# Kernel tuning notes

Hardware: AMD Instinct MI355X
Metric: run time of the kernel (lower is better)

## Reference

```python
import jax, jax.numpy as jnp
import numpy as np
import math

D_MODEL = 1024
N_HEADS = 16
D_HEAD = D_MODEL // N_HEADS
BIAS_HIDDEN = 32
B, N = 2, 1024


def setup_inputs() -> dict:
    key = jax.random.key(0)
    ks = jax.random.split(key, 16)
    s = 1.0 / math.sqrt(D_MODEL)
    inp = {
        "x": jax.random.normal(ks[0], (B, N, D_MODEL), dtype=jnp.float32),
        "xyz": jax.random.normal(ks[1], (B, N, 3), dtype=jnp.float32),
        "Wq": jax.random.normal(ks[2], (D_MODEL, D_MODEL), jnp.float32) * s,
        "bq": jnp.zeros((D_MODEL,), jnp.float32),
        "Wk": jax.random.normal(ks[3], (D_MODEL, D_MODEL), jnp.float32) * s,
        "bk": jnp.zeros((D_MODEL,), jnp.float32),
        "Wv": jax.random.normal(ks[4], (D_MODEL, D_MODEL), jnp.float32) * s,
        "bv": jnp.zeros((D_MODEL,), jnp.float32),
        "Wo": jax.random.normal(ks[5], (D_MODEL, D_MODEL), jnp.float32) * s,
        "bo": jnp.zeros((D_MODEL,), jnp.float32),
        "W1": jax.random.normal(ks[6], (3, BIAS_HIDDEN), jnp.float32) * (1.0 / math.sqrt(3.0)),
        "b1": jnp.zeros((BIAS_HIDDEN,), jnp.float32),
        "W2": jax.random.normal(ks[7], (BIAS_HIDDEN, N_HEADS), jnp.float32) * (1.0 / math.sqrt(BIAS_HIDDEN)),
        "b2": jnp.zeros((N_HEADS,), jnp.float32),
    }
    return inp


def reference(x, xyz, Wq, bq, Wk, bk, Wv, bv, Wo, bo, W1, b1, W2, b2):
    Bv, Nv, _ = x.shape
    # q,k,v projections -> [B, H, N, Dh]
    def proj(W, b):
        return (x @ W + b).reshape(Bv, Nv, N_HEADS, D_HEAD).transpose(0, 2, 1, 3)
    q = proj(Wq, bq)
    k = proj(Wk, bk)
    v = proj(Wv, bv)
    scores = jnp.einsum('bhid,bhjd->bhij', q, k) / math.sqrt(D_HEAD)
    # pairwise relative positions -> per-head bias via tiny MLP
    rel_pos = xyz[:, :, None, :] - xyz[:, None, :, :]            # [B,N,N,3]
    hidden = jax.nn.relu(rel_pos @ W1 + b1)                      # [B,N,N,hid]
    bias = (hidden @ W2 + b2).transpose(0, 3, 1, 2)              # [B,H,N,N]
    attn = jax.nn.softmax(scores + bias, axis=-1)                # [B,H,N,N]
    out = jnp.einsum('bhij,bhjd->bhid', attn, v)                 # [B,H,N,Dh]
    out = out.transpose(0, 2, 1, 3).reshape(Bv, Nv, D_MODEL)
    out = out @ Wo + bo
    return (out, attn)
```

## Files before the change

kernel.cpp:

```cpp
#include <hip/hip_runtime.h>
#include <hip/hip_bf16.h>
#include <math.h>

#define NTOK   1024
#define DMODEL 1024
#define NHEADS 16
#define DHEAD  64

typedef __attribute__((ext_vector_type(8))) short short8;
typedef __attribute__((ext_vector_type(4))) float floatx4;
#define MFMA(a,b,c) __builtin_amdgcn_mfma_f32_16x16x32_bf16(a,b,c,0,0,0)

__device__ __forceinline__ void bf16_split(float f, ushort& h, ushort& l) {
    unsigned u = __float_as_uint(f);
    unsigned hr = (u + 0x7FFFu + ((u >> 16) & 1u)) >> 16;
    h = (ushort)hr;
    float fh = __uint_as_float(hr << 16);
    float res = f - fh;
    unsigned u2 = __float_as_uint(res);
    l = (ushort)((u2 + 0x7FFFu + ((u2 >> 16) & 1u)) >> 16);
}

__device__ __forceinline__ int swzK(int r) { return (r & 7) ^ ((r >> 3) & 7); }

__global__ __launch_bounds__(256) void bias_kernel(
    const float* __restrict__ xyz,
    const float* __restrict__ W1, const float* __restrict__ b1,
    const float* __restrict__ W2, const float* __restrict__ b2,
    float* __restrict__ attnO)
{
    __shared__ float wbuf[656];
    int tid = threadIdx.x;
    for (int i = tid; i < 656; i += 256) {
        float v;
        if (i < 96)       v = W1[i];
        else if (i < 128) v = b1[i - 96];
        else if (i < 640) v = W2[i - 128];
        else              v = b2[i - 640];
        wbuf[i] = v;
    }
    __syncthreads();
    const float* w1s = wbuf;
    const float* b1s = wbuf + 96;
    const float* w2s = wbuf + 128;
    const float* b2s = wbuf + 640;

    int j = blockIdx.x * 256 + tid;
    int i = blockIdx.y;
    int b = blockIdx.z;

    float xi0 = xyz[((size_t)b * NTOK + i) * 3 + 0];
    float xi1 = xyz[((size_t)b * NTOK + i) * 3 + 1];
    float xi2 = xyz[((size_t)b * NTOK + i) * 3 + 2];
    float d0 = xi0 - xyz[((size_t)b * NTOK + j) * 3 + 0];
    float d1 = xi1 - xyz[((size_t)b * NTOK + j) * 3 + 1];
    float d2 = xi2 - xyz[((size_t)b * NTOK + j) * 3 + 2];

    float h[32];
#pragma unroll
    for (int hh = 0; hh < 32; ++hh) {
        float v = b1s[hh] + d0 * w1s[hh] + d1 * w1s[32 + hh] + d2 * w1s[64 + hh];
        h[hh] = fmaxf(v, 0.f);
    }
    size_t base = (size_t)b * NHEADS * 1048576 + (size_t)i * 1024 + j;
#pragma unroll
    for (int hd = 0; hd < NHEADS; ++hd) {
        float acc = b2s[hd];
#pragma unroll
        for (int hh = 0; hh < 32; ++hh) acc += h[hh] * w2s[hh * 16 + hd];
        attnO[base + (size_t)hd * 1048576] = acc;
    }
}

__global__ __launch_bounds__(256) void convx_kernel(
    const float* __restrict__ x, ushort* __restrict__ xh, ushort* __restrict__ xl)
{
    int id = blockIdx.x * 256 + threadIdx.x;
    float4 v = ((const float4*)x)[id];
    ushort h0,h1,h2,h3,l0,l1,l2,l3;
    bf16_split(v.x,h0,l0); bf16_split(v.y,h1,l1);
    bf16_split(v.z,h2,l2); bf16_split(v.w,h3,l3);
    ushort4 hv; hv.x=h0; hv.y=h1; hv.z=h2; hv.w=h3;
    ushort4 lv; lv.x=l0; lv.y=l1; lv.z=l2; lv.w=l3;
    ((ushort4*)xh)[id] = hv;
    ((ushort4*)xl)[id] = lv;
}

__global__ __launch_bounds__(256) void convw_kernel(
    const float* __restrict__ Wq, const float* __restrict__ Wk,
    const float* __restrict__ Wv, const float* __restrict__ Wo,
    ushort* __restrict__ Wcth, ushort* __restrict__ Wctl,
    ushort* __restrict__ Woth, ushort* __restrict__ Wotl)
{
    __shared__ float t[64][65];
    int z = blockIdx.z;
    const float* W = (z == 0) ? Wq : (z == 1) ? Wk : (z == 2) ? Wv : Wo;
    int n0 = blockIdx.x * 64, k0 = blockIdx.y * 64;
    int tid = threadIdx.x;
    int c4 = tid & 15, rr = tid >> 4;
#pragma unroll
    for (int t4 = 0; t4 < 4; ++t4) {
        int row = rr + t4 * 16;
        float4 v = *(const float4*)&W[(size_t)(k0 + row) * 1024 + n0 + c4 * 4];
        t[row][c4 * 4 + 0] = v.x; t[row][c4 * 4 + 1] = v.y;
        t[row][c4 * 4 + 2] = v.z; t[row][c4 * 4 + 3] = v.w;
    }
    __syncthreads();
    ushort* oh = (z < 3) ? Wcth : Woth;
    ushort* ol = (z < 3) ? Wctl : Wotl;
    int nbase = (z < 3) ? z * 1024 : 0;
#pragma unroll
    for (int t4 = 0; t4 < 4; ++t4) {
        int nl = rr + t4 * 16;
        int kk = c4 * 4;
        ushort4 hv, lv;
        ushort h, l;
        bf16_split(t[kk + 0][nl], h, l); hv.x = h; lv.x = l;
        bf16_split(t[kk + 1][nl], h, l); hv.y = h; lv.y = l;
        bf16_split(t[kk + 2][nl], h, l); hv.z = h; lv.z = l;
        bf16_split(t[kk + 3][nl], h, l); hv.w = h; lv.w = l;
        size_t o = (size_t)(nbase + n0 + nl) * 1024 + k0 + kk;
        *(ushort4*)&oh[o] = hv;
        *(ushort4*)&ol[o] = lv;
    }
}

__global__ __launch_bounds__(256) void mm_kernel(
    const ushort* __restrict__ Ah, const ushort* __restrict__ Al,
    const ushort* __restrict__ Bh, const ushort* __restrict__ Bl,
    const float* __restrict__ bq, const float* __restrict__ bk,
    const float* __restrict__ bv,
    float* __restrict__ out,
    ushort* __restrict__ qh, ushort* __restrict__ ql,
    ushort* __restrict__ kh, ushort* __restrict__ kl,
    ushort* __restrict__ vth, ushort* __restrict__ vtl,
    int mode)
{
    __shared__ ushort lds[4][64][64];

    int n0 = blockIdx.x * 64;
    int m0 = blockIdx.y * 64;
    int w = threadIdx.x >> 6, l = threadIdx.x & 63;
    int li = l & 15, lg = l >> 4;
    int wm = w >> 1, wn = w & 1;

    const ushort* gbase;
    if      (w == 0) gbase = Ah + (size_t)m0 * 1024;
    else if (w == 1) gbase = Al + (size_t)m0 * 1024;
    else if (w == 2) gbase = Bh + (size_t)n0 * 1024;
    else             gbase = Bl + (size_t)n0 * 1024;
    ushort* lbase = &lds[w][0][0];
    int srow = l >> 3;
    int sc   = l & 7;

    floatx4 acc[2][2];
#pragma unroll
    for (int i = 0; i < 2; ++i)
#pragma unroll
        for (int j = 0; j < 2; ++j) acc[i][j] = (floatx4){0.f, 0.f, 0.f, 0.f};

    for (int ks = 0; ks < 16; ++ks) {
        int k0 = ks * 64;
#pragma unroll
        for (int t = 0; t < 8; ++t) {
            int rl = t * 8 + srow;
            int cs = sc ^ swzK(rl);
            const ushort* g = gbase + (size_t)rl * 1024 + k0 + cs * 8;
            __builtin_amdgcn_global_load_lds(
                (const __attribute__((address_space(1))) unsigned int*)g,
                (__attribute__((address_space(3))) unsigned int*)(lbase + t * 512),
                16, 0, 0);
        }
        __syncthreads();
#pragma unroll
        for (int kk = 0; kk < 2; ++kk) {
            short8 a[2][2], b2[2][2];
#pragma unroll
            for (int f = 0; f < 2; ++f) {
                int ra = wm * 32 + f * 16 + li;
                int ca = ((kk * 4 + lg) ^ swzK(ra)) * 8;
                a[f][0] = *(const short8*)&lds[0][ra][ca];
                a[f][1] = *(const short8*)&lds[1][ra][ca];
                int rb = wn * 32 + f * 16 + li;
                int cb = ((kk * 4 + lg) ^ swzK(rb)) * 8;
                b2[f][0] = *(const short8*)&lds[2][rb][cb];
                b2[f][1] = *(const short8*)&lds[3][rb][cb];
            }
#pragma unroll
            for (int fm = 0; fm < 2; ++fm)
#pragma unroll
                for (int fn = 0; fn < 2; ++fn) {
                    acc[fm][fn] = MFMA(a[fm][0], b2[fn][0], acc[fm][fn]);
                    acc[fm][fn] = MFMA(a[fm][0], b2[fn][1], acc[fm][fn]);
                    acc[fm][fn] = MFMA(a[fm][1], b2[fn][0], acc[fm][fn]);
                }
        }
        __syncthreads();
    }

    if (mode == 0) {
#pragma unroll
        for (int fm = 0; fm < 2; ++fm)
#pragma unroll
            for (int fn = 0; fn < 2; ++fn) {
                int col = n0 + wn * 32 + fn * 16 + li;
                float bval = bq[col];
#pragma unroll
                for (int r = 0; r < 4; ++r) {
                    int row = m0 + wm * 32 + fm * 16 + lg * 4 + r;
                    out[(size_t)row * 1024 + col] = acc[fm][fn][r] + bval;
                }
            }
    } else {
        int z = n0 >> 10;
        const float* bp = (z == 0) ? bq : (z == 1) ? bk : bv;
#pragma unroll
        for (int fm = 0; fm < 2; ++fm)
#pragma unroll
            for (int fn = 0; fn < 2; ++fn) {
                int col = n0 + wn * 32 + fn * 16 + li;
                int nloc = col & 1023;
                int hd = nloc >> 6, d = nloc & 63;
                float bval = bp[nloc];
#pragma unroll
                for (int r = 0; r < 4; ++r) {
                    int row = m0 + wm * 32 + fm * 16 + lg * 4 + r;
                    int b = row >> 10, nn = row & 1023;
                    int bh = b * NHEADS + hd;
                    float v = acc[fm][fn][r] + bval;
                    ushort h, lo; bf16_split(v, h, lo);
                    if (z == 0) {
                        size_t o = ((size_t)bh * NTOK + nn) * DHEAD + d;
                        qh[o] = h; ql[o] = lo;
                    } else if (z == 1) {
                        size_t o = ((size_t)bh * NTOK + nn) * DHEAD + d;
                        kh[o] = h; kl[o] = lo;
                    } else {
                        size_t o = ((size_t)bh * DHEAD + d) * NTOK + nn;
                        vth[o] = h; vtl[o] = lo;
                    }
                }
            }
    }
}

__global__ __launch_bounds__(256) void score_kernel(
    const ushort* __restrict__ qh, const ushort* __restrict__ ql,
    const ushort* __restrict__ kh, const ushort* __restrict__ kl,
    float* __restrict__ attnO)
{
    __shared__ float redM[4][16];
    __shared__ float redS[4][16];
    int qt = blockIdx.x, hd = blockIdx.y, b = blockIdx.z;
    int bh = b * NHEADS + hd;
    int w = threadIdx.x >> 6, l = threadIdx.x & 63;
    int li = l & 15, lg = l >> 4;

    size_t qoff = ((size_t)bh * NTOK + qt * 16 + li) * DHEAD + lg * 8;
    short8 q0h = *(const short8*)(qh + qoff);
    short8 q0l = *(const short8*)(ql + qoff);
    short8 q1h = *(const short8*)(qh + qoff + 32);
    short8 q1l = *(const short8*)(ql + qoff + 32);

    floatx4 acc[16];
#pragma unroll
    for (int jf = 0; jf < 16; ++jf) acc[jf] = (floatx4){0.f, 0.f, 0.f, 0.f};

    int jbase = w * 256;
#pragma unroll
    for (int jf = 0; jf < 16; ++jf) {
        size_t koff = ((size_t)bh * NTOK + jbase + jf * 16 + li) * DHEAD + lg * 8;
        short8 K0h = *(const short8*)(kh + koff);
        short8 K0l = *(const short8*)(kl + koff);
        short8 K1h = *(const short8*)(kh + koff + 32);
        short8 K1l = *(const short8*)(kl + koff + 32);
        acc[jf] = MFMA(q0h, K0h, acc[jf]);
        acc[jf] = MFMA(q0h, K0l, acc[jf]);
        acc[jf] = MFMA(q0l, K0h, acc[jf]);
        acc[jf] = MFMA(q1h, K1h, acc[jf]);
        acc[jf] = MFMA(q1h, K1l, acc[jf]);
        acc[jf] = MFMA(q1l, K1h, acc[jf]);
    }

    float* prow = attnO + ((size_t)bh * NTOK + qt * 16) * NTOK;

    float mloc[4] = {-1e30f, -1e30f, -1e30f, -1e30f};
#pragma unroll
    for (int jf = 0; jf < 16; ++jf)
#pragma unroll
        for (int r = 0; r < 4; ++r) {
            float s = acc[jf][r] * 0.125f
                    + prow[(size_t)(lg * 4 + r) * NTOK + jbase + jf * 16 + li];
            acc[jf][r] = s;
            mloc[r] = fmaxf(mloc[r], s);
        }
#pragma unroll
    for (int r = 0; r < 4; ++r) {
        float m = mloc[r];
        m = fmaxf(m, __shfl_xor(m, 1, 64));
        m = fmaxf(m, __shfl_xor(m, 2, 64));
        m = fmaxf(m, __shfl_xor(m, 4, 64));
        m = fmaxf(m, __shfl_xor(m, 8, 64));
        mloc[r] = m;
    }
    if (li == 0) {
#pragma unroll
        for (int r = 0; r < 4; ++r) redM[w][lg * 4 + r] = mloc[r];
    }
    __syncthreads();
    float M[4];
#pragma unroll
    for (int r = 0; r < 4; ++r) {
        int row = lg * 4 + r;
        M[r] = fmaxf(fmaxf(redM[0][row], redM[1][row]),
                     fmaxf(redM[2][row], redM[3][row]));
    }
    float sloc[4] = {0.f, 0.f, 0.f, 0.f};
#pragma unroll
    for (int jf = 0; jf < 16; ++jf)
#pragma unroll
        for (int r = 0; r < 4; ++r) {
            float e = __expf(acc[jf][r] - M[r]);
            acc[jf][r] = e;
            sloc[r] += e;
        }
#pragma unroll
    for (int r = 0; r < 4; ++r) {
        float s = sloc[r];
        s += __shfl_xor(s, 1, 64);
        s += __shfl_xor(s, 2, 64);
        s += __shfl_xor(s, 4, 64);
        s += __shfl_xor(s, 8, 64);
        sloc[r] = s;
    }
    if (li == 0) {
#pragma unroll
        for (int r = 0; r < 4; ++r) redS[w][lg * 4 + r] = sloc[r];
    }
    __syncthreads();
    float inv[4];
#pragma unroll
    for (int r = 0; r < 4; ++r) {
        int row = lg * 4 + r;
        inv[r] = 1.0f / (redS[0][row] + redS[1][row] + redS[2][row] + redS[3][row]);
    }
#pragma unroll
    for (int jf = 0; jf < 16; ++jf)
#pragma unroll
        for (int r = 0; r < 4; ++r)
            prow[(size_t)(lg * 4 + r) * NTOK + jbase + jf * 16 + li] = acc[jf][r] * inv[r];
}

__global__ __launch_bounds__(256) void pv_kernel(
    const float* __restrict__ attnP,
    const ushort* __restrict__ vth, const ushort* __restrict__ vtl,
    ushort* __restrict__ awh, ushort* __restrict__ awl)
{
    int mt = blockIdx.x;
    int bh = blockIdx.y;
    int b = bh >> 4, hd = bh & 15;
    int w = threadIdx.x >> 6, l = threadIdx.x & 63;
    int li = l & 15, lg = l >> 4;
    int mrow = mt * 128 + w * 32;

    const float* P0 = attnP + ((size_t)bh * NTOK + mrow + li) * NTOK;
    const float* P1 = attnP + ((size_t)bh * NTOK + mrow + 16 + li) * NTOK;
    const ushort* v0h = vth + ((size_t)bh * DHEAD +  0 + li) * NTOK;
    const ushort* v1h = vth + ((size_t)bh * DHEAD + 16 + li) * NTOK;
    const ushort* v2h = vth + ((size_t)bh * DHEAD + 32 + li) * NTOK;
    const ushort* v3h = vth + ((size_t)bh * DHEAD + 48 + li) * NTOK;
    const ushort* v0l = vtl + ((size_t)bh * DHEAD +  0 + li) * NTOK;
    const ushort* v1l = vtl + ((size_t)bh * DHEAD + 16 + li) * NTOK;
    const ushort* v2l = vtl + ((size_t)bh * DHEAD + 32 + li) * NTOK;
    const ushort* v3l = vtl + ((size_t)bh * DHEAD + 48 + li) * NTOK;

    floatx4 acc[2][4];
#pragma unroll
    for (int i = 0; i < 2; ++i)
#pragma unroll
        for (int j = 0; j < 4; ++j) acc[i][j] = (floatx4){0.f, 0.f, 0.f, 0.f};

    for (int ks = 0; ks < 32; ++ks) {
        int ko = ks * 32 + lg * 8;
        float pa[8], pb[8];
        {
            float4 t0 = *(const float4*)(P0 + ko);
            float4 t1 = *(const float4*)(P0 + ko + 4);
            pa[0]=t0.x; pa[1]=t0.y; pa[2]=t0.z; pa[3]=t0.w;
            pa[4]=t1.x; pa[5]=t1.y; pa[6]=t1.z; pa[7]=t1.w;
            float4 t2 = *(const float4*)(P1 + ko);
            float4 t3 = *(const float4*)(P1 + ko + 4);
            pb[0]=t2.x; pb[1]=t2.y; pb[2]=t2.z; pb[3]=t2.w;
            pb[4]=t3.x; pb[5]=t3.y; pb[6]=t3.z; pb[7]=t3.w;
        }
        short8 A0h, A0l, A1h, A1l;
#pragma unroll
        for (int e = 0; e < 8; ++e) {
            ushort h, lo;
            bf16_split(pa[e], h, lo); A0h[e] = (short)h; A0l[e] = (short)lo;
            bf16_split(pb[e], h, lo); A1h[e] = (short)h; A1l[e] = (short)lo;
        }
#pragma unroll
        for (int nf = 0; nf < 4; ++nf) {
            const ushort* vhp = (nf == 0) ? v0h : (nf == 1) ? v1h : (nf == 2) ? v2h : v3h;
            const ushort* vlp = (nf == 0) ? v0l : (nf == 1) ? v1l : (nf == 2) ? v2l : v3l;
            short8 Bh8 = *(const short8*)(vhp + ko);
            short8 Bl8 = *(const short8*)(vlp + ko);
            acc[0][nf] = MFMA(A0h, Bh8, acc[0][nf]);
            acc[0][nf] = MFMA(A0h, Bl8, acc[0][nf]);
            acc[0][nf] = MFMA(A0l, Bh8, acc[0][nf]);
            acc[1][nf] = MFMA(A1h, Bh8, acc[1][nf]);
            acc[1][nf] = MFMA(A1h, Bl8, acc[1][nf]);
            acc[1][nf] = MFMA(A1l, Bh8, acc[1][nf]);
        }
    }
#pragma unroll
    for (int fm = 0; fm < 2; ++fm)
#pragma unroll
        for (int nf = 0; nf < 4; ++nf)
#pragma unroll
            for (int r = 0; r < 4; ++r) {
                int token = mrow + fm * 16 + lg * 4 + r;
                int d = nf * 16 + li;
                float v = acc[fm][nf][r];
                ushort h, lo; bf16_split(v, h, lo);
                size_t o = ((size_t)(b * NTOK + token)) * DMODEL + hd * DHEAD + d;
                awh[o] = h; awl[o] = lo;
            }
}

extern "C" void kernel_launch(void* const* d_in, const int* in_sizes, int n_in,
                              void* d_out, int out_size, void* d_ws, size_t ws_size,
                              hipStream_t stream)
{
    const float* x   = (const float*)d_in[0];
    const float* xyz = (const float*)d_in[1];
    const float* Wq  = (const float*)d_in[2];
    const float* bq  = (const float*)d_in[3];
    const float* Wk  = (const float*)d_in[4];
    const float* bk  = (const float*)d_in[5];
    const float* Wv  = (const float*)d_in[6];
    const float* bv  = (const float*)d_in[7];
    const float* Wo  = (const float*)d_in[8];
    const float* bo  = (const float*)d_in[9];
    const float* W1  = (const float*)d_in[10];
    const float* b1  = (const float*)d_in[11];
    const float* W2  = (const float*)d_in[12];
    const float* b2  = (const float*)d_in[13];

    const size_t OUT_ELEMS = (size_t)2 * NTOK * DMODEL;
    float* out   = (float*)d_out;
    float* attnO = out + OUT_ELEMS;

    char* ws = (char*)d_ws;
    ushort* Wcth = (ushort*)(ws);
    ushort* Wctl = (ushort*)(ws + 6291456);
    ushort* Woth = (ushort*)(ws + 12582912);
    ushort* Wotl = (ushort*)(ws + 14680064);
    ushort* qh   = (ushort*)(ws + 16777216);
    ushort* ql   = (ushort*)(ws + 20971520);
    ushort* kh   = (ushort*)(ws + 25165824);
    ushort* kl   = (ushort*)(ws + 29360128);
    ushort* vth  = (ushort*)(ws + 33554432);
    ushort* vtl  = (ushort*)(ws + 37748736);
    ushort* xh   = (ushort*)(ws + 41943040);
    ushort* xl   = (ushort*)(ws + 46137344);
    ushort* awh  = xh;
    ushort* awl  = xl;

    bias_kernel<<<dim3(4, 1024, 2), 256, 0, stream>>>(xyz, W1, b1, W2, b2, attnO);
    convx_kernel<<<dim3(2048), 256, 0, stream>>>(x, xh, xl);
    convw_kernel<<<dim3(16, 16, 4), 256, 0, stream>>>(Wq, Wk, Wv, Wo,
                                                      Wcth, Wctl, Woth, Wotl);
    mm_kernel<<<dim3(48, 32), 256, 0, stream>>>(xh, xl, Wcth, Wctl,
                                                bq, bk, bv, nullptr,
                                                qh, ql, kh, kl, vth, vtl, 1);
    score_kernel<<<dim3(64, NHEADS, 2), 256, 0, stream>>>(qh, ql, kh, kl, attnO);
    pv_kernel<<<dim3(8, 32), 256, 0, stream>>>(attnO, vth, vtl, awh, awl);
    mm_kernel<<<dim3(16, 32), 256, 0, stream>>>(awh, awl, Woth, Wotl,
                                                bo, bo, bo, out,
                                                nullptr, nullptr, nullptr, nullptr,
                                                nullptr, nullptr, 0);
}
```

Before: 427.8 us.

## Fuse softmax score kernel with P@V into a single attention kernel

Merges the score/softmax kernel and the separate P@V kernel. Normalized probabilities stay in registers, are split to bf16 hi/lo in shared memory, and are multiplied against V in the same block. Each wave handles a 256-key slice, and the four partial outputs are reduced through shared memory before the bf16 split store. This removes re-reading the full fp32 attention matrix from global memory and one launch. In exchange it uses much more shared memory per block and reloads V once per 16-row query tile rather than amortising it over 128 rows.

```diff
diff --git a/kernel.cpp b/kernel.cpp
--- a/kernel.cpp
+++ b/kernel.cpp
@@ -244,17 +244,25 @@
     }
 }
 
-__global__ __launch_bounds__(256) void score_kernel(
+__global__ __launch_bounds__(256) void attn_fused_kernel(
     const ushort* __restrict__ qh, const ushort* __restrict__ ql,
     const ushort* __restrict__ kh, const ushort* __restrict__ kl,
-    float* __restrict__ attnO)
-{
-    __shared__ float redM[4][16];
-    __shared__ float redS[4][16];
+    const ushort* __restrict__ vth, const ushort* __restrict__ vtl,
+    float* __restrict__ attnO,
+    ushort* __restrict__ awh, ushort* __restrict__ awl)
+{
+    __shared__ char smem[35328];
+    float* obuf = (float*)smem;
+    float* redM = (float*)(smem + 34816);
+    float* redS = (float*)(smem + 35072);
+
     int qt = blockIdx.x, hd = blockIdx.y, b = blockIdx.z;
     int bh = b * NHEADS + hd;
     int w = threadIdx.x >> 6, l = threadIdx.x & 63;
     int li = l & 15, lg = l >> 4;
+
+    ushort* pbh = (ushort*)smem + (size_t)w * 4352;
+    ushort* pbl = pbh + 2176;
 
     size_t qoff = ((size_t)bh * NTOK + qt * 16 + li) * DHEAD + lg * 8;
     short8 q0h = *(const short8*)(qh + qoff);
@@ -305,15 +313,15 @@
     }
     if (li == 0) {
 #pragma unroll
-        for (int r = 0; r < 4; ++r) redM[w][lg * 4 + r] = mloc[r];
+        for (int r = 0; r < 4; ++r) redM[w * 16 + lg * 4 + r] = mloc[r];
     }
     __syncthreads();
     float M[4];
 #pragma unroll
     for (int r = 0; r < 4; ++r) {
         int row = lg * 4 + r;
-        M[r] = fmaxf(fmaxf(redM[0][row], redM[1][row]),
-                     fmaxf(redM[2][row], redM[3][row]));
+        M[r] = fmaxf(fmaxf(redM[0 + row], redM[16 + row]),
+                     fmaxf(redM[32 + row], redM[48 + row]));
     }
     float sloc[4] = {0.f, 0.f, 0.f, 0.f};
 #pragma unroll
@@ -335,98 +343,86 @@
     }
     if (li == 0) {
 #pragma unroll
-        for (int r = 0; r < 4; ++r) redS[w][lg * 4 + r] = sloc[r];
+        for (int r = 0; r < 4; ++r) redS[w * 16 + lg * 4 + r] = sloc[r];
     }
     __syncthreads();
     float inv[4];
 #pragma unroll
     for (int r = 0; r < 4; ++r) {
         int row = lg * 4 + r;
-        inv[r] = 1.0f / (redS[0][row] + redS[1][row] + redS[2][row] + redS[3][row]);
+        inv[r] = 1.0f / (redS[0 + row] + redS[16 + row] +
+                         redS[32 + row] + redS[48 + row]);
     }
 #pragma unroll
     for (int jf = 0; jf < 16; ++jf)
 #pragma unroll
+        for (int r = 0; r < 4; ++r) {
+            float p = acc[jf][r] * inv[r];
+            acc[jf][r] = p;
+            prow[(size_t)(lg * 4 + r) * NTOK + jbase + jf * 16 + li] = p;
+        }
+
+    const ushort* vbh = vth + (size_t)bh * DHEAD * NTOK;
+    const ushort* vbl = vtl + (size_t)bh * DHEAD * NTOK;
+    floatx4 accv[4];
+#pragma unroll
+    for (int nf = 0; nf < 4; ++nf) accv[nf] = (floatx4){0.f, 0.f, 0.f, 0.f};
+
+#pragma unroll
+    for (int c = 0; c < 2; ++c) {
+#pragma unroll
+        for (int jf8 = 0; jf8 < 8; ++jf8) {
+            int jf = c * 8 + jf8;
+            int kloc = jf8 * 16 + li;
+#pragma unroll
+            for (int r = 0; r < 4; ++r) {
+                int row = lg * 4 + r;
+                ushort hh, ll; bf16_split(acc[jf][r], hh, ll);
+                pbh[row * 136 + kloc] = hh;
+                pbl[row * 136 + kloc] = ll;
+            }
+        }
+#pragma unroll
+        for (int ks = 0; ks < 4; ++ks) {
+            int koff_l = ks * 32 + lg * 8;
+            short8 Ah8 = *(const short8*)&pbh[li * 136 + koff_l];
+            short8 Al8 = *(const short8*)&pbl[li * 136 + koff_l];
+            size_t kg = (size_t)jbase + c * 128 + koff_l;
+#pragma unroll
+            for (int nf = 0; nf < 4; ++nf) {
+                short8 Bh8 = *(const short8*)(vbh + (size_t)(nf * 16 + li) * NTOK + kg);
+                short8 Bl8 = *(const short8*)(vbl + (size_t)(nf * 16 + li) * NTOK + kg);
+                accv[nf] = MFMA(Ah8, Bh8, accv[nf]);
+                accv[nf] = MFMA(Ah8, Bl8, accv[nf]);
+                accv[nf] = MFMA(Al8, Bh8, accv[nf]);
+            }
+        }
+    }
+
+    __syncthreads();
+#pragma unroll
+    for (int nf = 0; nf < 4; ++nf)
+#pragma unroll
         for (int r = 0; r < 4; ++r)
-            prow[(size_t)(lg * 4 + r) * NTOK + jbase + jf * 16 + li] = acc[jf][r] * inv[r];
-}
-
-__global__ __launch_bounds__(256) void pv_kernel(
-    const float* __restrict__ attnP,
-    const ushort* __restrict__ vth, const ushort* __restrict__ vtl,
-    ushort* __restrict__ awh, ushort* __restrict__ awl)
-{
-    int mt = blockIdx.x;
-    int bh = blockIdx.y;
-    int b = bh >> 4, hd = bh & 15;
-    int w = threadIdx.x >> 6, l = threadIdx.x & 63;
-    int li = l & 15, lg = l >> 4;
-    int mrow = mt * 128 + w * 32;
-
-    const float* P0 = attnP + ((size_t)bh * NTOK + mrow + li) * NTOK;
-    const float* P1 = attnP + ((size_t)bh * NTOK + mrow + 16 + li) * NTOK;
-    const ushort* v0h = vth + ((size_t)bh * DHEAD +  0 + li) * NTOK;
-    const ushort* v1h = vth + ((size_t)bh * DHEAD + 16 + li) * NTOK;
-    const ushort* v2h = vth + ((size_t)bh * DHEAD + 32 + li) * NTOK;
-    const ushort* v3h = vth + ((size_t)bh * DHEAD + 48 + li) * NTOK;
-    const ushort* v0l = vtl + ((size_t)bh * DHEAD +  0 + li) * NTOK;
-    const ushort* v1l = vtl + ((size_t)bh * DHEAD + 16 + li) * NTOK;
-    const ushort* v2l = vtl + ((size_t)bh * DHEAD + 32 + li) * NTOK;
-    const ushort* v3l = vtl + ((size_t)bh * DHEAD + 48 + li) * NTOK;
-
-    floatx4 acc[2][4];
-#pragma unroll
-    for (int i = 0; i < 2; ++i)
-#pragma unroll
-        for (int j = 0; j < 4; ++j) acc[i][j] = (floatx4){0.f, 0.f, 0.f, 0.f};
-
-    for (int ks = 0; ks < 32; ++ks) {
-        int ko = ks * 32 + lg * 8;
-        float pa[8], pb[8];
-        {
-            float4 t0 = *(const float4*)(P0 + ko);
-            float4 t1 = *(const float4*)(P0 + ko + 4);
-            pa[0]=t0.x; pa[1]=t0.y; pa[2]=t0.z; pa[3]=t0.w;
-            pa[4]=t1.x; pa[5]=t1.y; pa[6]=t1.z; pa[7]=t1.w;
-            float4 t2 = *(const float4*)(P1 + ko);
-            float4 t3 = *(const float4*)(P1 + ko + 4);
-            pb[0]=t2.x; pb[1]=t2.y; pb[2]=t2.z; pb[3]=t2.w;
-            pb[4]=t3.x; pb[5]=t3.y; pb[6]=t3.z; pb[7]=t3.w;
-        }
-        short8 A0h, A0l, A1h, A1l;
-#pragma unroll
-        for (int e = 0; e < 8; ++e) {
-            ushort h, lo;
-            bf16_split(pa[e], h, lo); A0h[e] = (short)h; A0l[e] = (short)lo;
-            bf16_split(pb[e], h, lo); A1h[e] = (short)h; A1l[e] = (short)lo;
-        }
-#pragma unroll
-        for (int nf = 0; nf < 4; ++nf) {
-            const ushort* vhp = (nf == 0) ? v0h : (nf == 1) ? v1h : (nf == 2) ? v2h : v3h;
-            const ushort* vlp = (nf == 0) ? v0l : (nf == 1) ? v1l : (nf == 2) ? v2l : v3l;
-            short8 Bh8 = *(const short8*)(vhp + ko);
-            short8 Bl8 = *(const short8*)(vlp + ko);
-            acc[0][nf] = MFMA(A0h, Bh8, acc[0][nf]);
-            acc[0][nf] = MFMA(A0h, Bl8, acc[0][nf]);
-            acc[0][nf] = MFMA(A0l, Bh8, acc[0][nf]);
-            acc[1][nf] = MFMA(A1h, Bh8, acc[1][nf]);
-            acc[1][nf] = MFMA(A1h, Bl8, acc[1][nf]);
-            acc[1][nf] = MFMA(A1l, Bh8, acc[1][nf]);
-        }
-    }
-#pragma unroll
-    for (int fm = 0; fm < 2; ++fm)
-#pragma unroll
-        for (int nf = 0; nf < 4; ++nf)
-#pragma unroll
-            for (int r = 0; r < 4; ++r) {
-                int token = mrow + fm * 16 + lg * 4 + r;
-                int d = nf * 16 + li;
-                float v = acc[fm][nf][r];
-                ushort h, lo; bf16_split(v, h, lo);
-                size_t o = ((size_t)(b * NTOK + token)) * DMODEL + hd * DHEAD + d;
-                awh[o] = h; awl[o] = lo;
-            }
+            obuf[(w * 16 + lg * 4 + r) * 68 + nf * 16 + li] = accv[nf][r];
+    __syncthreads();
+    {
+        int row = threadIdx.x >> 4, d0 = (threadIdx.x & 15) * 4;
+        float s0 = 0.f, s1 = 0.f, s2 = 0.f, s3 = 0.f;
+#pragma unroll
+        for (int ww = 0; ww < 4; ++ww) {
+            float4 t = *(const float4*)&obuf[(ww * 16 + row) * 68 + d0];
+            s0 += t.x; s1 += t.y; s2 += t.z; s3 += t.w;
+        }
+        ushort4 hv, lv; ushort h, lo;
+        bf16_split(s0, h, lo); hv.x = h; lv.x = lo;
+        bf16_split(s1, h, lo); hv.y = h; lv.y = lo;
+        bf16_split(s2, h, lo); hv.z = h; lv.z = lo;
+        bf16_split(s3, h, lo); hv.w = h; lv.w = lo;
+        size_t o = ((size_t)(b * NTOK + qt * 16 + row)) * DMODEL + hd * DHEAD + d0;
+        *(ushort4*)&awh[o] = hv;
+        *(ushort4*)&awl[o] = lv;
+    }
 }
 
 extern "C" void kernel_launch(void* const* d_in, const int* in_sizes, int n_in,
@@ -475,8 +471,8 @@
     mm_kernel<<<dim3(48, 32), 256, 0, stream>>>(xh, xl, Wcth, Wctl,
                                                 bq, bk, bv, nullptr,
                                                 qh, ql, kh, kl, vth, vtl, 1);
-    score_kernel<<<dim3(64, NHEADS, 2), 256, 0, stream>>>(qh, ql, kh, kl, attnO);
-    pv_kernel<<<dim3(8, 32), 256, 0, stream>>>(attnO, vth, vtl, awh, awl);
+    attn_fused_kernel<<<dim3(64, NHEADS, 2), 256, 0, stream>>>(
+        qh, ql, kh, kl, vth, vtl, attnO, awh, awl);
     mm_kernel<<<dim3(16, 32), 256, 0, stream>>>(awh, awl, Woth, Wotl,
                                                 bo, bo, bo, out,
                                                 nullptr, nullptr, nullptr, nullptr,
```

Measured after the change: 441.1 us. +3.1%, slower.
